# Kernel tuning notes

Hardware: AMD Instinct MI355X
Metric: run time of the kernel (lower is better)

Reference implementation:

```python
import jax, jax.numpy as jnp
import numpy as np

B, S, L, K, E, V = 2048, 4, 16, 8, 256, 128  # batch, max_steps, tokens/step, landmarks/cell, emb_sz, vocab


def setup_inputs() -> dict:
    key = jax.random.key(0)
    ks = jax.random.split(key, 10)
    std = 1.0 / (E * 9)
    return {
        "gold_table": jax.random.normal(ks[0], (11, E), jnp.float32),
        "map_table": jax.random.normal(ks[1], (V, E), jnp.float32) * 0.01,  # init_std=0.01
        "conv_weight": jax.random.uniform(ks[2], (E, E, 3, 3), jnp.float32, -std, std),
        "action_table": jax.random.normal(ks[3], (4, 32), jnp.float32),
        "action_W": jax.random.normal(ks[4], (9, 32), jnp.float32) * (1.0 / np.sqrt(32.0)),
        "action_b": jnp.zeros((9,), jnp.float32),
        "goldstandard": jax.random.randint(ks[5], (B, S, L), 0, 11),
        "actions": jax.random.randint(ks[6], (B, S - 1), 0, 4),
        "landmarks": jax.random.randint(ks[7], (B, 4, 4, K), 0, V),
        "y": jax.random.randint(ks[8], (B, 2), 0, 4),
    }


def _extract_patches(x):
    # x: [B,E,4,4] -> [B,9,E,16]; 3x3 neighborhoods with zero padding (conv padding=1)
    xp = jnp.pad(x, ((0, 0), (0, 0), (1, 1), (1, 1)))
    shifts = [xp[:, :, dh:dh + 4, dw:dw + 4].reshape(x.shape[0], x.shape[1], 16)
              for dh in range(3) for dw in range(3)]
    return jnp.stack(shifts, axis=1)


def reference(gold_table, map_table, conv_weight, action_table, action_W, action_b,
              goldstandard, actions, landmarks, y):
    Bn = y.shape[0]
    # goldstandard features: per-step embed+sum over tokens, concat over steps -> [B, S*E]
    emb = gold_table[goldstandard].sum(axis=2).reshape(Bn, -1)
    # MapEmbedding2d with padding_idx=0: zero row 0, embed, sum over landmark list
    mt = map_table.at[0].set(0.0)
    l_emb = mt[landmarks].sum(axis=3).transpose(0, 3, 1, 2)  # [B,E,4,4]
    # action-conditioned 3x3 masks, one per action
    action_out = action_table @ action_W.T + action_b  # [4,9]
    masks = jax.nn.softmax(action_out, axis=1)  # [4,9]
    Wr = conv_weight.reshape(E, E, 9)  # [O,I,tap]
    l_embs = [l_emb]
    cur = l_emb
    for j in range(S - 1):
        # per-sample routed mask == dispatch-to-expert conv; fused gather+masked-conv+scatter
        m = masks[actions[:, j]]  # [B,9]
        patches = _extract_patches(cur)  # [B,9,E,16]
        out = jnp.einsum('btip,bt,oit->bop', patches, m, Wr).reshape(Bn, E, 4, 4)
        l_embs.append(out)
        cur = out
    lm = jnp.concatenate(l_embs, axis=1).reshape(Bn, S * E, 16)  # [B, S*E, 16]
    logits = jnp.einsum('bcp,bc->bp', lm, emb)  # bmm(landmarks^T, emb)
    prob = jax.nn.softmax(logits, axis=1)
    y_true = y[:, 0] * 4 + y[:, 1]
    # torch CrossEntropyLoss applied to prob (softmax twice, as in the original)
    logp = jax.nn.log_softmax(prob, axis=1)
    loss = -jnp.take_along_axis(logp, y_true[:, None], axis=1).mean()
    acc = (jnp.argmax(prob, axis=1) == y_true).astype(jnp.float32).mean()
    return loss, acc, prob
```

## Files before the change

### kernel.cpp

```cpp
#include <hip/hip_runtime.h>
#include <hip/hip_bf16.h>

typedef __attribute__((ext_vector_type(4))) float f32x4;
typedef __attribute__((ext_vector_type(8))) short short8;

#define NB 2048

__device__ __forceinline__ float bf2f(ushort u) {
    union { unsigned int u; float f; } x; x.u = ((unsigned int)u) << 16; return x.f;
}
__device__ __forceinline__ ushort f2bf(float f) {
    union { float f; unsigned int u; } x; x.f = f;
    unsigned int u = x.u;
    unsigned int r = (u + 0x7fffu + ((u >> 16) & 1u)) >> 16;
    return (ushort)r;
}

__global__ __launch_bounds__(256) void k_prep(
    const float* __restrict__ conv_w, const float* __restrict__ a_table,
    const float* __restrict__ a_W, const float* __restrict__ a_b,
    float* __restrict__ masks, ushort* __restrict__ Wg,
    float* __restrict__ out_head)
{
    __shared__ float ao[4][9];
    const int bid = blockIdx.x, tid = threadIdx.x;
    if (bid == 256) {
        if (tid < 36) {
            const int a = tid / 9, t = tid % 9;
            float s = a_b[t];
            for (int c = 0; c < 32; c++) s += a_table[a * 32 + c] * a_W[t * 32 + c];
            ao[a][t] = s;
        }
        __syncthreads();
        if (tid < 4) {
            float mx = -1e30f;
            for (int t = 0; t < 9; t++) mx = fmaxf(mx, ao[tid][t]);
            float e[9], z = 0.f;
            for (int t = 0; t < 9; t++) { e[t] = expf(ao[tid][t] - mx); z += e[t]; }
            for (int t = 0; t < 9; t++) masks[tid * 9 + t] = e[t] / z;
        }
        if (tid == 64) { out_head[0] = 0.f; out_head[1] = 0.f; }
    } else {
        const int o = bid;
        for (int q = 0; q < 9; q++) {
            const float v = conv_w[(o * 256 + tid) * 9 + q];
            Wg[o * 2304 + q * 256 + tid] = f2bf(v);
        }
    }
}

__global__ __launch_bounds__(256) void k_emb(
    const float* __restrict__ gold, const int* __restrict__ gs,
    float* __restrict__ emb)
{
    const int bs = blockIdx.x, e = threadIdx.x;
    const int* g = gs + bs * 16;
    float s = 0.f;
    #pragma unroll
    for (int l = 0; l < 16; l++) s += gold[g[l] * 256 + e];
    emb[bs * 256 + e] = s;
}

__global__ __launch_bounds__(256) void k_lemb(
    const float* __restrict__ mapt, const int* __restrict__ lms,
    float* __restrict__ lp32, ushort* __restrict__ c0)
{
    const int b = blockIdx.x, e = threadIdx.x;
    for (int p = 0; p < 16; p++) {
        const int* lm = lms + (b * 16 + p) * 8;
        float s = 0.f;
        #pragma unroll
        for (int k = 0; k < 8; k++) {
            const int idx = lm[k];
            if (idx) s += mapt[idx * 256 + e];
        }
        lp32[(b * 16 + p) * 256 + e] = s;
        c0[(b * 16 + p) * 256 + e] = f2bf(s);
    }
}

__global__ __launch_bounds__(256) void k_conv(
    const ushort* __restrict__ cur, const ushort* __restrict__ Wg,
    const float* __restrict__ masks, const int* __restrict__ actions,
    const int j, ushort* __restrict__ outp)
{
    __shared__ __align__(16) ushort Wlds[256][48];
    __shared__ __align__(16) ushort Xlds[64][48];
    __shared__ float mlds[4][9];
    const int tid = threadIdx.x;
    const int b0 = blockIdx.x * 4;
    if (tid < 36) {
        const int s = tid / 9, t = tid % 9;
        mlds[s][t] = masks[actions[(b0 + s) * 3 + j] * 9 + t];
    }
    const int wid = tid >> 6, lane = tid & 63;
    const int l15 = lane & 15, l4 = lane >> 4;
    const int xc = tid >> 2, xq = tid & 3;
    const int xs = xc >> 4, xp = xc & 15;
    const int xh = xp >> 2, xw = xp & 3;
    const ushort* curb = cur + (size_t)(b0 + xs) * 16 * 256;
    const ushort* wrow = Wg + tid * 2304;

    f32x4 acc[4][4];
    #pragma unroll
    for (int a = 0; a < 4; a++)
        #pragma unroll
        for (int b = 0; b < 4; b++) acc[a][b] = (f32x4){0.f, 0.f, 0.f, 0.f};

    uint4 xv, w0, w1, w2, w3;
    auto load_tile = [&](int k0) {
        const int t = k0 >> 8, i0 = k0 & 255;
        const int hh = xh + t / 3 - 1, ww = xw + t % 3 - 1;
        xv = make_uint4(0u, 0u, 0u, 0u);
        if (hh >= 0 && hh < 4 && ww >= 0 && ww < 4) {
            const ushort* src = curb + ((hh << 2) + ww) * 256 + i0 + xq * 8;
            uint4 v = *(const uint4*)src;
            const float mm = mlds[xs][t];
            const ushort* vi = (const ushort*)&v;
            ushort* vo = (ushort*)&xv;
            #pragma unroll
            for (int e = 0; e < 8; e++) vo[e] = f2bf(bf2f(vi[e]) * mm);
        }
        w0 = *(const uint4*)(wrow + k0);
        w1 = *(const uint4*)(wrow + k0 + 8);
        w2 = *(const uint4*)(wrow + k0 + 16);
        w3 = *(const uint4*)(wrow + k0 + 24);
    };

    __syncthreads();
    load_tile(0);
    for (int k0 = 0; k0 < 2304; k0 += 32) {
        __syncthreads();
        *(uint4*)&Xlds[xc][xq * 8] = xv;
        *(uint4*)&Wlds[tid][0]  = w0;
        *(uint4*)&Wlds[tid][8]  = w1;
        *(uint4*)&Wlds[tid][16] = w2;
        *(uint4*)&Wlds[tid][24] = w3;
        __syncthreads();
        if (k0 + 32 < 2304) load_tile(k0 + 32);
        short8 af[4], bfr[4];
        #pragma unroll
        for (int mt = 0; mt < 4; mt++)
            af[mt] = *(const short8*)&Wlds[wid * 64 + mt * 16 + l15][l4 * 8];
        #pragma unroll
        for (int nt = 0; nt < 4; nt++)
            bfr[nt] = *(const short8*)&Xlds[nt * 16 + l15][l4 * 8];
        #pragma unroll
        for (int mt = 0; mt < 4; mt++)
            #pragma unroll
            for (int nt = 0; nt < 4; nt++)
                acc[mt][nt] = __builtin_amdgcn_mfma_f32_16x16x32_bf16(
                    af[mt], bfr[nt], acc[mt][nt], 0, 0, 0);
    }
    #pragma unroll
    for (int nt = 0; nt < 4; nt++) {
        const size_t bb = (size_t)(b0 + nt);
        #pragma unroll
        for (int mt = 0; mt < 4; mt++) {
            const int ob = wid * 64 + mt * 16 + l4 * 4;
            ushort o4[4];
            #pragma unroll
            for (int r = 0; r < 4; r++) o4[r] = f2bf(acc[mt][nt][r]);
            *(uint2*)&outp[(bb * 16 + l15) * 256 + ob] = *(const uint2*)o4;
        }
    }
}

__global__ __launch_bounds__(256) void k_final(
    const float* __restrict__ lp32, const ushort* __restrict__ c1,
    const ushort* __restrict__ c2, const ushort* __restrict__ c3,
    const float* __restrict__ emb, const int* __restrict__ y,
    float* __restrict__ d_out)
{
    __shared__ float red[256];
    __shared__ float lg[16];
    const int b = blockIdx.x, tid = threadIdx.x;
    const int p = tid >> 4, g = tid & 15;
    const float* embb = emb + b * 1024;
    float a = 0.f;
    {
        const float* row = lp32 + (size_t)(b * 16 + p) * 256;
        #pragma unroll 4
        for (int q = 0; q < 16; q++) { const int e = g + q * 16; a += row[e] * embb[e]; }
    }
    const ushort* cs[3] = { c1, c2, c3 };
    for (int s = 1; s < 4; s++) {
        const ushort* row = cs[s - 1] + (size_t)(b * 16 + p) * 256;
        const float* eb = embb + s * 256;
        #pragma unroll 4
        for (int q = 0; q < 16; q++) { const int e = g + q * 16; a += bf2f(row[e]) * eb[e]; }
    }
    red[tid] = a;
    __syncthreads();
    for (int st = 8; st >= 1; st >>= 1) {
        if (g < st) red[tid] += red[tid + st];
        __syncthreads();
    }
    if (g == 0) lg[p] = red[tid];
    __syncthreads();
    if (tid == 0) {
        float mx = -1e30f;
        for (int q = 0; q < 16; q++) mx = fmaxf(mx, lg[q]);
        float ex[16], z = 0.f;
        for (int q = 0; q < 16; q++) { ex[q] = expf(lg[q] - mx); z += ex[q]; }
        float prob[16];
        for (int q = 0; q < 16; q++) {
            prob[q] = ex[q] / z;
            d_out[2 + b * 16 + q] = prob[q];
        }
        int am = 0; float bv = prob[0];
        for (int q = 1; q < 16; q++) if (prob[q] > bv) { bv = prob[q]; am = q; }
        const int yt = y[b * 2] * 4 + y[b * 2 + 1];
        float z2 = 0.f;
        for (int q = 0; q < 16; q++) z2 += expf(prob[q]);
        const float logp = prob[yt] - logf(z2);
        atomicAdd(&d_out[0], -logp * (1.0f / 2048.0f));
        atomicAdd(&d_out[1], (am == yt) ? (1.0f / 2048.0f) : 0.0f);
    }
}

extern "C" void kernel_launch(void* const* d_in, const int* in_sizes, int n_in,
                              void* d_out, int out_size, void* d_ws, size_t ws_size,
                              hipStream_t stream) {
    const float* gold_table = (const float*)d_in[0];
    const float* map_table  = (const float*)d_in[1];
    const float* conv_w     = (const float*)d_in[2];
    const float* a_table    = (const float*)d_in[3];
    const float* a_W        = (const float*)d_in[4];
    const float* a_b        = (const float*)d_in[5];
    const int*   gs         = (const int*)d_in[6];
    const int*   actions    = (const int*)d_in[7];
    const int*   lms        = (const int*)d_in[8];
    const int*   y          = (const int*)d_in[9];
    float* out = (float*)d_out;

    char* ws = (char*)d_ws;
    float*  masks = (float*)(ws + 0);
    ushort* Wg    = (ushort*)(ws + 256);
    float*  emb   = (float*)(ws + 1179904);
    float*  lp32  = (float*)(ws + 9568512);
    ushort* c0    = (ushort*)(ws + 43122944);
    ushort* c1    = (ushort*)(ws + 59900160);
    ushort* c2    = (ushort*)(ws + 76677376);
    ushort* c3    = (ushort*)(ws + 93454592);
    (void)in_sizes; (void)n_in; (void)out_size; (void)ws_size;

    k_prep<<<257, 256, 0, stream>>>(conv_w, a_table, a_W, a_b, masks, Wg, out);
    k_emb<<<8192, 256, 0, stream>>>(gold_table, gs, emb);
    k_lemb<<<2048, 256, 0, stream>>>(map_table, lms, lp32, c0);
    k_conv<<<512, 256, 0, stream>>>(c0, Wg, masks, actions, 0, c1);
    k_conv<<<512, 256, 0, stream>>>(c1, Wg, masks, actions, 1, c2);
    k_conv<<<512, 256, 0, stream>>>(c2, Wg, masks, actions, 2, c3);
    k_final<<<2048, 256, 0, stream>>>(lp32, c1, c2, c3, emb, y, out);
}
```

Before: 450.8 us.

## Fold action masks into per-action conv weights and bucket samples by action

Precomputes four mask-scaled bf16 weight copies and groups samples by action with an atomic bucketing kernel, so each conv workgroup runs a plain GEMM over one action's weights with no per-element masking. The conv kernel is retiled to load weight tiles with global_load_lds into swizzled, double-buffered LDS, with 64-wide K steps, and its workgroups are mapped to XCDs. It also fuses the gold embedding into the final kernel and drops the fp32 landmark copy, using bf16 c0 instead. This trades some precision, since step 0 and the mask-weight products are now rounded to bf16, and adds atomics plus extra launches and memsets.

```diff
diff --git a/kernel.cpp b/kernel.cpp
--- a/kernel.cpp
+++ b/kernel.cpp
@@ -3,8 +3,6 @@
 
 typedef __attribute__((ext_vector_type(4))) float f32x4;
 typedef __attribute__((ext_vector_type(8))) short short8;
-
-#define NB 2048
 
 __device__ __forceinline__ float bf2f(ushort u) {
     union { unsigned int u; float f; } x; x.u = ((unsigned int)u) << 16; return x.f;
@@ -15,55 +13,58 @@
     unsigned int r = (u + 0x7fffu + ((u >> 16) & 1u)) >> 16;
     return (ushort)r;
 }
-
-__global__ __launch_bounds__(256) void k_prep(
+__device__ __forceinline__ void gload16(const ushort* g, ushort* l) {
+    __builtin_amdgcn_global_load_lds(
+        (const __attribute__((address_space(1))) unsigned int*)g,
+        (__attribute__((address_space(3))) unsigned int*)l, 16, 0, 0);
+}
+
+__global__ __launch_bounds__(256) void k_wfold(
     const float* __restrict__ conv_w, const float* __restrict__ a_table,
     const float* __restrict__ a_W, const float* __restrict__ a_b,
-    float* __restrict__ masks, ushort* __restrict__ Wg,
-    float* __restrict__ out_head)
+    ushort* __restrict__ Wa)
 {
     __shared__ float ao[4][9];
-    const int bid = blockIdx.x, tid = threadIdx.x;
-    if (bid == 256) {
-        if (tid < 36) {
-            const int a = tid / 9, t = tid % 9;
-            float s = a_b[t];
-            for (int c = 0; c < 32; c++) s += a_table[a * 32 + c] * a_W[t * 32 + c];
-            ao[a][t] = s;
-        }
-        __syncthreads();
-        if (tid < 4) {
-            float mx = -1e30f;
-            for (int t = 0; t < 9; t++) mx = fmaxf(mx, ao[tid][t]);
-            float e[9], z = 0.f;
-            for (int t = 0; t < 9; t++) { e[t] = expf(ao[tid][t] - mx); z += e[t]; }
-            for (int t = 0; t < 9; t++) masks[tid * 9 + t] = e[t] / z;
-        }
-        if (tid == 64) { out_head[0] = 0.f; out_head[1] = 0.f; }
-    } else {
-        const int o = bid;
-        for (int q = 0; q < 9; q++) {
-            const float v = conv_w[(o * 256 + tid) * 9 + q];
-            Wg[o * 2304 + q * 256 + tid] = f2bf(v);
-        }
-    }
-}
-
-__global__ __launch_bounds__(256) void k_emb(
-    const float* __restrict__ gold, const int* __restrict__ gs,
-    float* __restrict__ emb)
-{
-    const int bs = blockIdx.x, e = threadIdx.x;
-    const int* g = gs + bs * 16;
-    float s = 0.f;
-    #pragma unroll
-    for (int l = 0; l < 16; l++) s += gold[g[l] * 256 + e];
-    emb[bs * 256 + e] = s;
+    __shared__ float m[4][9];
+    const int o = blockIdx.x, tid = threadIdx.x;
+    if (tid < 36) {
+        const int a = tid / 9, t = tid % 9;
+        float s = a_b[t];
+        for (int c = 0; c < 32; c++) s += a_table[a * 32 + c] * a_W[t * 32 + c];
+        ao[a][t] = s;
+    }
+    __syncthreads();
+    if (tid < 4) {
+        float mx = -1e30f;
+        for (int t = 0; t < 9; t++) mx = fmaxf(mx, ao[tid][t]);
+        float e[9], z = 0.f;
+        for (int t = 0; t < 9; t++) { e[t] = expf(ao[tid][t] - mx); z += e[t]; }
+        for (int t = 0; t < 9; t++) m[tid][t] = e[t] / z;
+    }
+    __syncthreads();
+    float w9[9];
+    #pragma unroll
+    for (int t = 0; t < 9; t++) w9[t] = conv_w[(o * 256 + tid) * 9 + t];
+    #pragma unroll
+    for (int a = 0; a < 4; a++)
+        #pragma unroll
+        for (int t = 0; t < 9; t++)
+            Wa[(size_t)((a << 8) + o) * 2304 + t * 256 + tid] = f2bf(m[a][t] * w9[t]);
+}
+
+__global__ __launch_bounds__(256) void k_bucket(
+    const int* __restrict__ actions, int* __restrict__ cnt, int* __restrict__ list)
+{
+    const int idx = blockIdx.x * 256 + threadIdx.x;
+    const int j = idx >> 11, b = idx & 2047;
+    const int a = actions[b * 3 + j];
+    const int pos = atomicAdd(&cnt[j * 4 + a], 1);
+    list[((j * 4 + a) << 11) + pos] = b;
 }
 
 __global__ __launch_bounds__(256) void k_lemb(
     const float* __restrict__ mapt, const int* __restrict__ lms,
-    float* __restrict__ lp32, ushort* __restrict__ c0)
+    ushort* __restrict__ c0)
 {
     const int b = blockIdx.x, e = threadIdx.x;
     for (int p = 0; p < 16; p++) {
@@ -74,129 +75,169 @@
             const int idx = lm[k];
             if (idx) s += mapt[idx * 256 + e];
         }
-        lp32[(b * 16 + p) * 256 + e] = s;
-        c0[(b * 16 + p) * 256 + e] = f2bf(s);
-    }
-}
-
-__global__ __launch_bounds__(256) void k_conv(
-    const ushort* __restrict__ cur, const ushort* __restrict__ Wg,
-    const float* __restrict__ masks, const int* __restrict__ actions,
+        c0[(size_t)(b * 16 + p) * 256 + e] = f2bf(s);
+    }
+}
+
+__global__ __launch_bounds__(256, 2) void k_conv(
+    const ushort* __restrict__ cur, const ushort* __restrict__ Wa,
+    const int* __restrict__ cnt, const int* __restrict__ list,
     const int j, ushort* __restrict__ outp)
 {
-    __shared__ __align__(16) ushort Wlds[256][48];
-    __shared__ __align__(16) ushort Xlds[64][48];
-    __shared__ float mlds[4][9];
+    __shared__ __align__(16) ushort Alds[2][256 * 64];
     const int tid = threadIdx.x;
-    const int b0 = blockIdx.x * 4;
-    if (tid < 36) {
-        const int s = tid / 9, t = tid % 9;
-        mlds[s][t] = masks[actions[(b0 + s) * 3 + j] * 9 + t];
-    }
+
+    const int c0n = cnt[j * 4 + 0], c1n = cnt[j * 4 + 1],
+              c2n = cnt[j * 4 + 2], c3n = cnt[j * 4 + 3];
+    const int t0 = (c0n + 3) >> 2;
+    const int t1 = t0 + ((c1n + 3) >> 2);
+    const int t2 = t1 + ((c2n + 3) >> 2);
+    const int t3 = t2 + ((c3n + 3) >> 2);
+    const int bid = blockIdx.x;
+    const int xcd = bid & 7, sub = bid >> 3;
+    const int wg = (xcd < 4 ? xcd * 65 : 260 + (xcd - 4) * 64) + sub;
+    if (wg >= t3) return;
+    int a, off, ca;
+    if      (wg < t0) { a = 0; off = 0;  ca = c0n; }
+    else if (wg < t1) { a = 1; off = t0; ca = c1n; }
+    else if (wg < t2) { a = 2; off = t1; ca = c2n; }
+    else              { a = 3; off = t2; ca = c3n; }
+    const int slot0 = (wg - off) * 4;
+    const int* la = list + ((j * 4 + a) << 11);
+    const ushort* wbase = Wa + (size_t)(a << 8) * 2304;
+
     const int wid = tid >> 6, lane = tid & 63;
     const int l15 = lane & 15, l4 = lane >> 4;
-    const int xc = tid >> 2, xq = tid & 3;
-    const int xs = xc >> 4, xp = xc & 15;
-    const int xh = xp >> 2, xw = xp & 3;
-    const ushort* curb = cur + (size_t)(b0 + xs) * 16 * 256;
-    const ushort* wrow = Wg + tid * 2304;
-
-    f32x4 acc[4][4];
-    #pragma unroll
-    for (int a = 0; a < 4; a++)
-        #pragma unroll
-        for (int b = 0; b < 4; b++) acc[a][b] = (f32x4){0.f, 0.f, 0.f, 0.f};
-
-    uint4 xv, w0, w1, w2, w3;
-    auto load_tile = [&](int k0) {
+    const int wm = wid >> 1, wn = wid & 1;
+
+    int sid[2]; bool vst[2];
+    #pragma unroll
+    for (int nf = 0; nf < 2; nf++) {
+        const int sl = slot0 + wn * 2 + nf;
+        vst[nf] = sl < ca;
+        sid[nf] = vst[nf] ? la[sl] : 0;
+    }
+
+    const int srow = tid >> 3, sc = tid & 7;
+    const int wubase = (tid & ~63) * 8;
+    #define STAGE(buf, k0)                                                     \
+        _Pragma("unroll")                                                      \
+        for (int qq = 0; qq < 8; qq++) {                                       \
+            const int row = qq * 32 + srow;                                    \
+            const int cc = sc ^ (row & 7);                                     \
+            gload16(wbase + (size_t)row * 2304 + (k0) + cc * 8,                \
+                    &Alds[buf][qq * 2048 + wubase]);                           \
+        }
+
+    f32x4 acc[8][2];
+    #pragma unroll
+    for (int mf = 0; mf < 8; mf++) {
+        acc[mf][0] = (f32x4){0.f, 0.f, 0.f, 0.f};
+        acc[mf][1] = (f32x4){0.f, 0.f, 0.f, 0.f};
+    }
+
+    const short8 bzero = {0, 0, 0, 0, 0, 0, 0, 0};
+    const int ph = l15 >> 2, pw = l15 & 3;
+    STAGE(0, 0);
+
+    int cb = 0;
+    for (int ks = 0; ks < 36; ks++) {
+        const int k0 = ks * 64;
         const int t = k0 >> 8, i0 = k0 & 255;
-        const int hh = xh + t / 3 - 1, ww = xw + t % 3 - 1;
-        xv = make_uint4(0u, 0u, 0u, 0u);
-        if (hh >= 0 && hh < 4 && ww >= 0 && ww < 4) {
-            const ushort* src = curb + ((hh << 2) + ww) * 256 + i0 + xq * 8;
-            uint4 v = *(const uint4*)src;
-            const float mm = mlds[xs][t];
-            const ushort* vi = (const ushort*)&v;
-            ushort* vo = (ushort*)&xv;
+        const int hh = ph + t / 3 - 1, ww = pw + t % 3 - 1;
+        const bool xv = (hh >= 0) & (hh < 4) & (ww >= 0) & (ww < 4);
+        const int psrc = (hh << 2) + ww;
+
+        __syncthreads();
+
+        short8 bfr[2][2];
+        #pragma unroll
+        for (int nf = 0; nf < 2; nf++)
             #pragma unroll
-            for (int e = 0; e < 8; e++) vo[e] = f2bf(bf2f(vi[e]) * mm);
-        }
-        w0 = *(const uint4*)(wrow + k0);
-        w1 = *(const uint4*)(wrow + k0 + 8);
-        w2 = *(const uint4*)(wrow + k0 + 16);
-        w3 = *(const uint4*)(wrow + k0 + 24);
-    };
-
-    __syncthreads();
-    load_tile(0);
-    for (int k0 = 0; k0 < 2304; k0 += 32) {
-        __syncthreads();
-        *(uint4*)&Xlds[xc][xq * 8] = xv;
-        *(uint4*)&Wlds[tid][0]  = w0;
-        *(uint4*)&Wlds[tid][8]  = w1;
-        *(uint4*)&Wlds[tid][16] = w2;
-        *(uint4*)&Wlds[tid][24] = w3;
-        __syncthreads();
-        if (k0 + 32 < 2304) load_tile(k0 + 32);
-        short8 af[4], bfr[4];
-        #pragma unroll
-        for (int mt = 0; mt < 4; mt++)
-            af[mt] = *(const short8*)&Wlds[wid * 64 + mt * 16 + l15][l4 * 8];
-        #pragma unroll
-        for (int nt = 0; nt < 4; nt++)
-            bfr[nt] = *(const short8*)&Xlds[nt * 16 + l15][l4 * 8];
-        #pragma unroll
-        for (int mt = 0; mt < 4; mt++)
+            for (int kf = 0; kf < 2; kf++) {
+                const int i = i0 + kf * 32 + l4 * 8;
+                const ushort* src = cur + ((size_t)sid[nf] * 16 + psrc) * 256 + i;
+                bfr[nf][kf] = xv ? *(const short8*)src : bzero;
+            }
+
+        if (ks + 1 < 36) STAGE(cb ^ 1, k0 + 64);
+
+        #pragma unroll
+        for (int kf = 0; kf < 2; kf++) {
             #pragma unroll
-            for (int nt = 0; nt < 4; nt++)
-                acc[mt][nt] = __builtin_amdgcn_mfma_f32_16x16x32_bf16(
-                    af[mt], bfr[nt], acc[mt][nt], 0, 0, 0);
-    }
-    #pragma unroll
-    for (int nt = 0; nt < 4; nt++) {
-        const size_t bb = (size_t)(b0 + nt);
-        #pragma unroll
-        for (int mt = 0; mt < 4; mt++) {
-            const int ob = wid * 64 + mt * 16 + l4 * 4;
+            for (int mf = 0; mf < 8; mf++) {
+                const int rr = wm * 128 + mf * 16 + l15;
+                const int cc = (kf * 4 + l4) ^ (rr & 7);
+                const short8 af = *(const short8*)&Alds[cb][rr * 64 + cc * 8];
+                acc[mf][0] = __builtin_amdgcn_mfma_f32_16x16x32_bf16(
+                    af, bfr[0][kf], acc[mf][0], 0, 0, 0);
+                acc[mf][1] = __builtin_amdgcn_mfma_f32_16x16x32_bf16(
+                    af, bfr[1][kf], acc[mf][1], 0, 0, 0);
+            }
+        }
+        cb ^= 1;
+    }
+
+    #pragma unroll
+    for (int nf = 0; nf < 2; nf++) {
+        if (!vst[nf]) continue;
+        const size_t rowb = ((size_t)sid[nf] * 16 + l15) * 256;
+        #pragma unroll
+        for (int mf = 0; mf < 8; mf++) {
+            const int ob = wm * 128 + mf * 16 + l4 * 4;
             ushort o4[4];
             #pragma unroll
-            for (int r = 0; r < 4; r++) o4[r] = f2bf(acc[mt][nt][r]);
-            *(uint2*)&outp[(bb * 16 + l15) * 256 + ob] = *(const uint2*)o4;
-        }
-    }
+            for (int r = 0; r < 4; r++) o4[r] = f2bf(acc[mf][nf][r]);
+            *(uint2*)&outp[rowb + ob] = *(const uint2*)o4;
+        }
+    }
+    #undef STAGE
 }
 
 __global__ __launch_bounds__(256) void k_final(
-    const float* __restrict__ lp32, const ushort* __restrict__ c1,
+    const ushort* __restrict__ c0, const ushort* __restrict__ c1,
     const ushort* __restrict__ c2, const ushort* __restrict__ c3,
-    const float* __restrict__ emb, const int* __restrict__ y,
-    float* __restrict__ d_out)
-{
+    const float* __restrict__ gold, const int* __restrict__ gs,
+    const int* __restrict__ y, float* __restrict__ d_out)
+{
+    __shared__ float embl[4][256];
     __shared__ float red[256];
     __shared__ float lg[16];
     const int b = blockIdx.x, tid = threadIdx.x;
-    const int p = tid >> 4, g = tid & 15;
-    const float* embb = emb + b * 1024;
-    float a = 0.f;
     {
-        const float* row = lp32 + (size_t)(b * 16 + p) * 256;
+        const int s = tid >> 6, e0 = (tid & 63) * 4;
+        const int* g = gs + b * 64 + s * 16;
+        float4 accv = make_float4(0.f, 0.f, 0.f, 0.f);
+        #pragma unroll
+        for (int l = 0; l < 16; l++) {
+            const float4 v = *(const float4*)&gold[g[l] * 256 + e0];
+            accv.x += v.x; accv.y += v.y; accv.z += v.z; accv.w += v.w;
+        }
+        *(float4*)&embl[s][e0] = accv;
+    }
+    __syncthreads();
+    const int p = tid >> 4, g16 = tid & 15;
+    const ushort* rows[4] = {
+        c0 + (size_t)(b * 16 + p) * 256, c1 + (size_t)(b * 16 + p) * 256,
+        c2 + (size_t)(b * 16 + p) * 256, c3 + (size_t)(b * 16 + p) * 256 };
+    float acc = 0.f;
+    #pragma unroll
+    for (int s = 0; s < 4; s++) {
+        const ushort* row = rows[s];
+        const float* eb = embl[s];
         #pragma unroll 4
-        for (int q = 0; q < 16; q++) { const int e = g + q * 16; a += row[e] * embb[e]; }
-    }
-    const ushort* cs[3] = { c1, c2, c3 };
-    for (int s = 1; s < 4; s++) {
-        const ushort* row = cs[s - 1] + (size_t)(b * 16 + p) * 256;
-        const float* eb = embb + s * 256;
-        #pragma unroll 4
-        for (int q = 0; q < 16; q++) { const int e = g + q * 16; a += bf2f(row[e]) * eb[e]; }
-    }
-    red[tid] = a;
+        for (int q = 0; q < 16; q++) {
+            const int e = g16 + q * 16;
+            acc += bf2f(row[e]) * eb[e];
+        }
+    }
+    red[tid] = acc;
     __syncthreads();
     for (int st = 8; st >= 1; st >>= 1) {
-        if (g < st) red[tid] += red[tid + st];
+        if (g16 < st) red[tid] += red[tid + st];
         __syncthreads();
     }
-    if (g == 0) lg[p] = red[tid];
+    if (g16 == 0) lg[p] = red[tid];
     __syncthreads();
     if (tid == 0) {
         float mx = -1e30f;
@@ -235,21 +276,22 @@
     float* out = (float*)d_out;
 
     char* ws = (char*)d_ws;
-    float*  masks = (float*)(ws + 0);
-    ushort* Wg    = (ushort*)(ws + 256);
-    float*  emb   = (float*)(ws + 1179904);
-    float*  lp32  = (float*)(ws + 9568512);
-    ushort* c0    = (ushort*)(ws + 43122944);
-    ushort* c1    = (ushort*)(ws + 59900160);
-    ushort* c2    = (ushort*)(ws + 76677376);
-    ushort* c3    = (ushort*)(ws + 93454592);
+    int*    cnt  = (int*)(ws + 0);
+    int*    list = (int*)(ws + 256);
+    ushort* Wa   = (ushort*)(ws + 131072);
+    ushort* c0   = (ushort*)(ws + 4849664);
+    ushort* c1   = (ushort*)(ws + 21626880);
+    ushort* c2   = (ushort*)(ws + 38404096);
+    ushort* c3   = (ushort*)(ws + 55181312);
     (void)in_sizes; (void)n_in; (void)out_size; (void)ws_size;
 
-    k_prep<<<257, 256, 0, stream>>>(conv_w, a_table, a_W, a_b, masks, Wg, out);
-    k_emb<<<8192, 256, 0, stream>>>(gold_table, gs, emb);
-    k_lemb<<<2048, 256, 0, stream>>>(map_table, lms, lp32, c0);
-    k_conv<<<512, 256, 0, stream>>>(c0, Wg, masks, actions, 0, c1);
-    k_conv<<<512, 256, 0, stream>>>(c1, Wg, masks, actions, 1, c2);
-    k_conv<<<512, 256, 0, stream>>>(c2, Wg, masks, actions, 2, c3);
-    k_final<<<2048, 256, 0, stream>>>(lp32, c1, c2, c3, emb, y, out);
-}
+    hipMemsetAsync(cnt, 0, 48, stream);
+    hipMemsetAsync(d_out, 0, 2 * sizeof(float), stream);
+    k_wfold <<<256, 256, 0, stream>>>(conv_w, a_table, a_W, a_b, Wa);
+    k_bucket<<<24, 256, 0, stream>>>(actions, cnt, list);
+    k_lemb  <<<2048, 256, 0, stream>>>(map_table, lms, c0);
+    k_conv  <<<516, 256, 0, stream>>>(c0, Wa, cnt, list, 0, c1);
+    k_conv  <<<516, 256, 0, stream>>>(c1, Wa, cnt, list, 1, c2);
+    k_conv  <<<516, 256, 0, stream>>>(c2, Wa, cnt, list, 2, c3);
+    k_final <<<2048, 256, 0, stream>>>(c0, c1, c2, c3, gold_table, gs, y, out);
+}
```

New measurement: 494.2 us. +9.6%, slower.
